# Kernel tuning notes

Measured on AMD Instinct MI355X. Metric: run time of the kernel, lower is better.

## Reference

```python
import jax, jax.numpy as jnp
import numpy as np
from jax import lax

B, N, NPOINT, NSAMPLE = 8, 8192, 2048, 32
RADIUS = 0.2
D_FEAT = 64
MLP = [64, 64, 128]
IN_CH = 3 + D_FEAT
EPS = 1e-5


def setup_inputs() -> dict:
    key = jax.random.key(0)
    ks = jax.random.split(key, 2 + len(MLP))
    inp = {
        "xyz": jax.random.uniform(ks[0], (B, N, 3), dtype=jnp.float32),
        "points": jax.random.normal(ks[1], (B, N, D_FEAT), dtype=jnp.float32),
    }
    cin = IN_CH
    for i, cout in enumerate(MLP):
        inp[f"W{i+1}"] = jax.random.normal(ks[2 + i], (cout, cin), dtype=jnp.float32) * 0.05
        inp[f"b{i+1}"] = jnp.zeros((cout,), jnp.float32)
        inp[f"g{i+1}"] = jnp.ones((cout,), jnp.float32)
        inp[f"be{i+1}"] = jnp.zeros((cout,), jnp.float32)
        cin = cout
    return inp


def farthest_point_sample(xyz, npoint):
    # xyz: (B, N, 3) -> (B, npoint) int32 indices. Deterministic start at index 0.
    Bb, Nn, _ = xyz.shape
    barange = jnp.arange(Bb)

    def step(carry, _):
        distance, farthest = carry
        centroid = xyz[barange, farthest]                      # (B, 3)
        d = jnp.sum((xyz - centroid[:, None, :]) ** 2, -1)     # (B, N)
        distance = jnp.minimum(distance, d)
        new_far = jnp.argmax(distance, axis=-1).astype(jnp.int32)
        return (distance, new_far), farthest

    init = (jnp.full((Bb, Nn), 1e10, xyz.dtype), jnp.zeros((Bb,), jnp.int32))
    _, idxs = lax.scan(step, init, None, length=npoint)        # (npoint, B)
    return idxs.T                                              # (B, npoint)


def index_points(points, idx):
    # points: (B, N, C); idx: (B, S) or (B, S, K)
    return jax.vmap(lambda p, i: p[i])(points, idx)


def square_distance(src, dst):
    # (B, S, C) x (B, N, C) -> (B, S, N)
    d = -2.0 * jnp.einsum('bsc,bnc->bsn', src, dst)
    d += jnp.sum(src ** 2, -1)[:, :, None]
    d += jnp.sum(dst ** 2, -1)[:, None, :]
    return d


def query_ball_point(radius, nsample, xyz, new_xyz):
    Bb, Nn, _ = xyz.shape
    sqr = square_distance(new_xyz, xyz)                        # (B, S, N)
    grid = jnp.arange(Nn, dtype=jnp.int32)
    group_idx = jnp.where(sqr > radius * radius, Nn, grid)     # invalid -> N
    # nsample smallest indices == torch sort(dim=-1)[:, :, :nsample]
    neg_vals, _ = lax.top_k(-group_idx, nsample)               # (B, S, K)
    group_idx = -neg_vals
    first = group_idx[:, :, 0:1]
    return jnp.where(group_idx == Nn, first, group_idx)


def bn_relu(x, gamma, beta):
    # x: (B, C, L). Training-mode batchnorm (biased variance) + ReLU.
    mean = jnp.mean(x, axis=(0, 2), keepdims=True)
    var = jnp.mean((x - mean) ** 2, axis=(0, 2), keepdims=True)
    xn = (x - mean) * lax.rsqrt(var + EPS)
    return jax.nn.relu(xn * gamma[None, :, None] + beta[None, :, None])


def reference(xyz, points, W1, b1, g1, be1, W2, b2, g2, be2, W3, b3, g3, be3):
    Bb = xyz.shape[0]
    fps_idx = farthest_point_sample(xyz, NPOINT)               # (B, S)
    new_xyz = index_points(xyz, fps_idx)                       # (B, S, 3)
    idx = query_ball_point(RADIUS, NSAMPLE, xyz, new_xyz)      # (B, S, K)
    grouped_xyz = index_points(xyz, idx)                       # (B, S, K, 3)
    grouped_xyz_norm = grouped_xyz - new_xyz[:, :, None, :]
    grouped_points = index_points(points, idx)                 # (B, S, K, D)
    g = jnp.concatenate([grouped_xyz_norm, grouped_points], -1)  # (B, S, K, C)
    x = g.reshape(Bb, NPOINT * NSAMPLE, -1).transpose(0, 2, 1)   # (B, C, S*K)
    for W, b, ga, be in ((W1, b1, g1, be1), (W2, b2, g2, be2), (W3, b3, g3, be3)):
        x = jnp.einsum('oc,bcl->bol', W, x) + b[None, :, None]
        x = bn_relu(x, ga, be)
    x = x.reshape(Bb, -1, NPOINT, NSAMPLE)
    new_points = jnp.max(x, axis=-1).transpose(0, 2, 1)        # (B, S, C_out)
    return new_xyz, new_points
```

## Files before the change

kernel.cpp:

```cpp
#include <hip/hip_runtime.h>
#include <hip/hip_bf16.h>

#define NB 8
#define NN 8192
#define NP 2048
#define NS 32
#define INV_P (1.0f/524288.0f)

typedef float v2f __attribute__((ext_vector_type(2)));

template<int CTRL>
__device__ __forceinline__ float fmax_dpp(float v) {
  const int x = __builtin_amdgcn_update_dpp(0, __float_as_int(v), CTRL, 0xF, 0xF, true);
  return fmaxf(v, __int_as_float(x));
}


__global__ __launch_bounds__(512)
void k_fps_pre(const float* __restrict__ xyz, const float* __restrict__ feat,
               const float* __restrict__ W1, const float* __restrict__ b1,
               float* __restrict__ F, float* __restrict__ outXyz, float* __restrict__ stats)
{
#pragma clang fp contract(off)
  __shared__ union U { float4 xyzw[NN]; float fx[128*64]; } sh;
  __shared__ unsigned long long cand[2][8];
  const int t = threadIdx.x;
  if (blockIdx.x < 8) {
    const int b = blockIdx.x;
    const float* xb = xyz + (size_t)b*NN*3;
    v2f px[8], py[8], pz[8], dd[8];
#pragma unroll
    for (int j = 0; j < 8; ++j) {
      const int i0 = t*16 + 2*j;
      const float x0 = xb[i0*3+0], y0 = xb[i0*3+1], z0 = xb[i0*3+2];
      const float x1 = xb[i0*3+3], y1 = xb[i0*3+4], z1 = xb[i0*3+5];
      px[j] = (v2f){x0,x1}; py[j] = (v2f){y0,y1}; pz[j] = (v2f){z0,z1};
      dd[j] = (v2f){1e10f,1e10f};
      sh.xyzw[i0]   = make_float4(x0,y0,z0,0.f);
      sh.xyzw[i0+1] = make_float4(x1,y1,z1,0.f);
    }
    __syncthreads();
    const int lane = t & 63, wv = t >> 6;
    float4 cf = sh.xyzw[0];
    for (int s = 0; s < NP; ++s) {
      if (t == 0) {
        float* o = outXyz + ((size_t)b*NP+s)*3;
        o[0]=cf.x; o[1]=cf.y; o[2]=cf.z;
      }
      const v2f cx = {cf.x,cf.x}, cy = {cf.y,cf.y}, cz = {cf.z,cf.z};
      float m = -1.f; int mi = 0;
#pragma unroll
      for (int j = 0; j < 8; ++j) {
        const v2f dx = px[j]-cx, dy = py[j]-cy, dz = pz[j]-cz;
        v2f d = dx*dx; d = d + dy*dy; d = d + dz*dz;
        const float n0 = fminf(dd[j].x, d.x);
        const float n1 = fminf(dd[j].y, d.y);
        dd[j].x = n0; dd[j].y = n1;
        if (n0 > m) { m = n0; mi = 2*j;   }
        if (n1 > m) { m = n1; mi = 2*j+1; }
      }
      float r = m;
      r = fmax_dpp<0xB1>(r);
      r = fmax_dpp<0x4E>(r);
      r = fmax_dpp<0x141>(r);
      r = fmax_dpp<0x140>(r);
      r = fmax_dpp<0x142>(r);
      r = fmax_dpp<0x143>(r);
      const int wmb  = __builtin_amdgcn_readlane(__float_as_int(r), 63);
      const float wm = __int_as_float(wmb);
      const unsigned long long mk = __ballot(m == wm);
      const int ls  = __ffsll((long long)mk) - 1;
      const int miw = __builtin_amdgcn_readlane(mi, ls);
      const unsigned idx = (unsigned)((wv*64 + ls)*16 + miw);
      if (lane == 0)
        cand[s&1][wv] = ((unsigned long long)(unsigned)wmb << 32)
                      | (unsigned long long)(0xFFFFFFFFu - idx);
      __syncthreads();
      unsigned long long best = cand[s&1][0];
#pragma unroll
      for (int w = 1; w < 8; ++w) { const unsigned long long c = cand[s&1][w]; if (c > best) best = c; }
      const int far = (int)(0xFFFFFFFFu - (unsigned)(best & 0xFFFFFFFFull));
      cf = sh.xyzw[far];
    }
  } else {
    if (blockIdx.x == 8) {
      for (int i = t; i < 512*16; i += 512) stats[i] = 0.f;
    }
    const int blk = blockIdx.x - 8;
    const int base = blk * 128;
    const int b = base >> 13;
    const int n0 = base & (NN-1);
    {
      const int row = t >> 2, seg = t & 3;
      const float* src = feat + ((size_t)(b*NN + n0 + row))*64 + seg*16;
#pragma unroll
      for (int k = 0; k < 4; ++k) {
        const float4 v = *(const float4*)(src + k*4);
        *(float4*)&sh.fx[row*64 + seg*16 + k*4] = v;
      }
    }
    __syncthreads();
    const int o = t & 63, wv = t >> 6;
    float w[64];
#pragma unroll
    for (int c = 0; c < 64; ++c) w[c] = W1[o*67 + 3 + c];
    const float bb = b1[o];
    for (int r = wv*16; r < wv*16+16; ++r) {
      float acc = bb;
#pragma unroll
      for (int c4 = 0; c4 < 16; ++c4) {
        const float4 xq = *(const float4*)&sh.fx[r*64 + c4*4];
        acc = fmaf(w[c4*4+0], xq.x, acc);
        acc = fmaf(w[c4*4+1], xq.y, acc);
        acc = fmaf(w[c4*4+2], xq.z, acc);
        acc = fmaf(w[c4*4+3], xq.w, acc);
      }
      F[((size_t)(b*NN + n0 + r))*64 + o] = acc;
    }
  }
}

__global__ __launch_bounds__(256)
void k_ball(const float* __restrict__ xyz, const float* __restrict__ newXyz,
            const float* __restrict__ F, const float* __restrict__ W1,
            __hip_bfloat16* __restrict__ y1, float* __restrict__ stats)
{
  __shared__ float xs[NN], ys[NN], zs[NN];
  __shared__ int sel[4][NS];
  const int t = threadIdx.x;
  const int b = blockIdx.x >> 5;
  const int chunk = blockIdx.x & 31;
  const float* xb = xyz + (size_t)b*NN*3;
  for (int i = t; i < NN; i += 256) {
    xs[i] = xb[i*3+0]; ys[i] = xb[i*3+1]; zs[i] = xb[i*3+2];
  }
  __syncthreads();
  const int lane = t & 63, wv = t >> 6;
  const float w0 = W1[lane*67+0], w1 = W1[lane*67+1], w2 = W1[lane*67+2];
  const double rr = 0.2*0.2;
  float ls = 0.f, lq = 0.f;
  for (int qi = 0; qi < 16; ++qi) {
    const int q  = chunk*64 + wv*16 + qi;
    const int gq = b*NP + q;
    const float cx = newXyz[(size_t)gq*3+0], cy = newXyz[(size_t)gq*3+1], cz = newXyz[(size_t)gq*3+2];
    const double cxd = (double)cx, cyd = (double)cy, czd = (double)cz;
    const double ssd = cxd*cxd + cyd*cyd + czd*czd;
    int have = 0;
    for (int c0 = 0; c0 < NN; c0 += 64) {
      const int i = c0 + lane;
      const double x = (double)xs[i], y = (double)ys[i], z = (double)zs[i];
      const double dot = x*cxd + y*cyd + z*czd;
      const double pn2 = x*x + y*y + z*z;
      const double d = -2.0*dot + ssd + pn2;
      const bool ok = d <= rr;
      const unsigned long long mk = __ballot(ok);
      const int rank = __popcll(mk & ((1ull<<lane)-1ull));
      if (ok && have + rank < NS) sel[wv][have+rank] = i;
      have += (int)__popcll(mk);
      if (have >= NS) break;
    }
    if (have > NS) have = NS;
    const int first = sel[wv][0];
    if (lane >= have && lane < NS) sel[wv][lane] = first;
    for (int j = 0; j < NS; ++j) {
      const int i = sel[wv][j];
      const float dxn = xs[i]-cx, dyn = ys[i]-cy, dzn = zs[i]-cz;
      const float f = F[((size_t)(b*NN+i))*64 + lane];
      float yv = fmaf(w0,dxn,f); yv = fmaf(w1,dyn,yv); yv = fmaf(w2,dzn,yv);
      y1[((size_t)gq*NS + j)*64 + lane] = __float2bfloat16(yv);
      ls += yv; lq = fmaf(yv,yv,lq);
    }
  }
  atomicAdd(&stats[(0 +lane)*16], ls);
  atomicAdd(&stats[(64+lane)*16], lq);
}

__device__ inline void stage_bn(const __hip_bfloat16* __restrict__ src, float* __restrict__ xt,
                                const float* __restrict__ A, const float* __restrict__ Bc,
                                int t, int blockBase)
{
  const uint4* s = (const uint4*)(src + ((size_t)(blockBase + t))*64);
  float* row = &xt[t*64];
  const int sw = t & 7;
#pragma unroll
  for (int g = 0; g < 8; ++g) {
    const uint4 v = s[g];
    const unsigned uu[4] = {v.x, v.y, v.z, v.w};
    const float4 Aq0 = ((const float4*)A)[g*2],  Aq1 = ((const float4*)A)[g*2+1];
    const float4 Bq0 = ((const float4*)Bc)[g*2], Bq1 = ((const float4*)Bc)[g*2+1];
    float e[8];
#pragma unroll
    for (int k = 0; k < 4; ++k) {
      const float f0 = __uint_as_float(uu[k] << 16);
      const float f1 = __uint_as_float(uu[k] & 0xFFFF0000u);
      const float a0 = (k<2) ? ((k==0)?Aq0.x:Aq0.z) : ((k==2)?Aq1.x:Aq1.z);
      const float a1 = (k<2) ? ((k==0)?Aq0.y:Aq0.w) : ((k==2)?Aq1.y:Aq1.w);
      const float bb0 = (k<2) ? ((k==0)?Bq0.x:Bq0.z) : ((k==2)?Bq1.x:Bq1.z);
      const float bb1 = (k<2) ? ((k==0)?Bq0.y:Bq0.w) : ((k==2)?Bq1.y:Bq1.w);
      e[k*2+0] = fmaxf(fmaf(f0, a0, bb0), 0.f);
      e[k*2+1] = fmaxf(fmaf(f1, a1, bb1), 0.f);
    }
    const float4 q0 = make_float4(e[0],e[1],e[2],e[3]);
    const float4 q1 = make_float4(e[4],e[5],e[6],e[7]);
    ((float4*)row)[(g*2)   ^ sw] = q0;
    ((float4*)row)[(g*2+1) ^ sw] = q1;
  }
}

__global__ __launch_bounds__(256)
void k_l2(const __hip_bfloat16* __restrict__ y1, float* __restrict__ stats,
          const float* __restrict__ g1, const float* __restrict__ be1,
          const float* __restrict__ W2, const float* __restrict__ b2,
          __hip_bfloat16* __restrict__ y2)
{
  __shared__ float xt[256*64];
  __shared__ float A[64], Bc[64], ssh[64], qsh[64];
  const int t = threadIdx.x;
  if (t < 64) {
    const float mean = stats[t*16] * INV_P;
    float var = stats[(64+t)*16] * INV_P - mean*mean;
    if (var < 0.f) var = 0.f;
    const float rs = rsqrtf(var + 1e-5f);
    const float a = rs * g1[t];
    A[t] = a; Bc[t] = fmaf(-mean, a, be1[t]);
    ssh[t] = 0.f; qsh[t] = 0.f;
  }
  const int lane = t & 63, wv = t >> 6;
  float w[64];
#pragma unroll
  for (int c4 = 0; c4 < 16; ++c4) {
    const float4 v = *(const float4*)(W2 + lane*64 + c4*4);
    w[c4*4+0]=v.x; w[c4*4+1]=v.y; w[c4*4+2]=v.z; w[c4*4+3]=v.w;
  }
  const float bo = b2[lane];
  __syncthreads();
  stage_bn(y1, xt, A, Bc, t, blockIdx.x*256);
  __syncthreads();
  float ls = 0.f, lq = 0.f;
  for (int pp = 0; pp < 64; ++pp) {
    const int p = wv*64 + pp;
    const int sw = p & 7;
    const float* row = &xt[p*64];
    float acc = bo;
#pragma unroll
    for (int c4 = 0; c4 < 16; ++c4) {
      const float4 xq = ((const float4*)row)[c4 ^ sw];
      acc = fmaf(w[c4*4+0], xq.x, acc);
      acc = fmaf(w[c4*4+1], xq.y, acc);
      acc = fmaf(w[c4*4+2], xq.z, acc);
      acc = fmaf(w[c4*4+3], xq.w, acc);
    }
    y2[((size_t)(blockIdx.x*256 + p))*64 + lane] = __float2bfloat16(acc);
    ls += acc; lq = fmaf(acc,acc,lq);
  }
  atomicAdd(&ssh[lane], ls);
  atomicAdd(&qsh[lane], lq);
  __syncthreads();
  if (t < 64) {
    atomicAdd(&stats[(128+t)*16], ssh[t]);
    atomicAdd(&stats[(192+t)*16], qsh[t]);
  }
}

__global__ __launch_bounds__(256)
void k_l3stats(const __hip_bfloat16* __restrict__ y2, float* __restrict__ stats,
               const float* __restrict__ g2, const float* __restrict__ be2,
               const float* __restrict__ W3, const float* __restrict__ b3)
{
  __shared__ float xt[256*64];
  __shared__ float A[64], Bc[64], ssh[128], qsh[128];
  const int t = threadIdx.x;
  if (t < 64) {
    const float mean = stats[(128+t)*16] * INV_P;
    float var = stats[(192+t)*16] * INV_P - mean*mean;
    if (var < 0.f) var = 0.f;
    const float rs = rsqrtf(var + 1e-5f);
    const float a = rs * g2[t];
    A[t] = a; Bc[t] = fmaf(-mean, a, be2[t]);
  }
  if (t < 128) { ssh[t]=0.f; qsh[t]=0.f; }
  const int lane = t & 63, wv = t >> 6;
  float w0[64], w1[64];
#pragma unroll
  for (int c4 = 0; c4 < 16; ++c4) {
    const float4 v  = *(const float4*)(W3 + lane*64 + c4*4);
    const float4 v2 = *(const float4*)(W3 + (size_t)(lane+64)*64 + c4*4);
    w0[c4*4+0]=v.x;  w0[c4*4+1]=v.y;  w0[c4*4+2]=v.z;  w0[c4*4+3]=v.w;
    w1[c4*4+0]=v2.x; w1[c4*4+1]=v2.y; w1[c4*4+2]=v2.z; w1[c4*4+3]=v2.w;
  }
  const float bo0 = b3[lane], bo1 = b3[lane+64];
  __syncthreads();
  stage_bn(y2, xt, A, Bc, t, blockIdx.x*256);
  __syncthreads();
  float ls0=0.f,lq0=0.f,ls1=0.f,lq1=0.f;
  for (int pp = 0; pp < 64; ++pp) {
    const int p = wv*64 + pp;
    const int sw = p & 7;
    const float* row = &xt[p*64];
    float a0 = bo0, a1 = bo1;
#pragma unroll
    for (int c4 = 0; c4 < 16; ++c4) {
      const float4 xq = ((const float4*)row)[c4 ^ sw];
      a0 = fmaf(w0[c4*4+0], xq.x, a0); a0 = fmaf(w0[c4*4+1], xq.y, a0);
      a0 = fmaf(w0[c4*4+2], xq.z, a0); a0 = fmaf(w0[c4*4+3], xq.w, a0);
      a1 = fmaf(w1[c4*4+0], xq.x, a1); a1 = fmaf(w1[c4*4+1], xq.y, a1);
      a1 = fmaf(w1[c4*4+2], xq.z, a1); a1 = fmaf(w1[c4*4+3], xq.w, a1);
    }
    ls0 += a0; lq0 = fmaf(a0,a0,lq0);
    ls1 += a1; lq1 = fmaf(a1,a1,lq1);
  }
  atomicAdd(&ssh[lane], ls0);    atomicAdd(&qsh[lane], lq0);
  atomicAdd(&ssh[64+lane], ls1); atomicAdd(&qsh[64+lane], lq1);
  __syncthreads();
  if (t < 128) {
    atomicAdd(&stats[(256+t)*16], ssh[t]);
    atomicAdd(&stats[(384+t)*16], qsh[t]);
  }
}

__global__ __launch_bounds__(256)
void k_out(const __hip_bfloat16* __restrict__ y2, const float* __restrict__ stats,
           const float* __restrict__ g2, const float* __restrict__ be2,
           const float* __restrict__ W3, const float* __restrict__ b3,
           const float* __restrict__ g3, const float* __restrict__ be3,
           float* __restrict__ out)
{
  __shared__ float xt[256*64];
  __shared__ float A[64], Bc[64], A3[128], B3[128];
  const int t = threadIdx.x;
  if (t < 64) {
    const float mean = stats[(128+t)*16] * INV_P;
    float var = stats[(192+t)*16] * INV_P - mean*mean;
    if (var < 0.f) var = 0.f;
    const float rs = rsqrtf(var + 1e-5f);
    const float a = rs * g2[t];
    A[t] = a; Bc[t] = fmaf(-mean, a, be2[t]);
  }
  if (t < 128) {
    const float mean = stats[(256+t)*16] * INV_P;
    float var = stats[(384+t)*16] * INV_P - mean*mean;
    if (var < 0.f) var = 0.f;
    const float rs = rsqrtf(var + 1e-5f);
    const float a = rs * g3[t];
    A3[t] = a; B3[t] = fmaf(-mean, a, be3[t]);
  }
  const int lane = t & 63, wv = t >> 6;
  float w0[64], w1[64];
#pragma unroll
  for (int c4 = 0; c4 < 16; ++c4) {
    const float4 v  = *(const float4*)(W3 + lane*64 + c4*4);
    const float4 v2 = *(const float4*)(W3 + (size_t)(lane+64)*64 + c4*4);
    w0[c4*4+0]=v.x;  w0[c4*4+1]=v.y;  w0[c4*4+2]=v.z;  w0[c4*4+3]=v.w;
    w1[c4*4+0]=v2.x; w1[c4*4+1]=v2.y; w1[c4*4+2]=v2.z; w1[c4*4+3]=v2.w;
  }
  const float bo0 = b3[lane], bo1 = b3[lane+64];
  __syncthreads();
  stage_bn(y2, xt, A, Bc, t, blockIdx.x*256);
  __syncthreads();
  const float a3l0 = A3[lane], b3l0 = B3[lane];
  const float a3l1 = A3[64+lane], b3l1 = B3[64+lane];
  for (int which = 0; which < 2; ++which) {
    float mx0 = -1e30f, mx1 = -1e30f;
    for (int j = 0; j < 32; ++j) {
      const int p = (wv*2+which)*32 + j;
      const int sw = p & 7;
      const float* row = &xt[p*64];
      float a0 = bo0, a1 = bo1;
#pragma unroll
      for (int c4 = 0; c4 < 16; ++c4) {
        const float4 xq = ((const float4*)row)[c4 ^ sw];
        a0 = fmaf(w0[c4*4+0], xq.x, a0); a0 = fmaf(w0[c4*4+1], xq.y, a0);
        a0 = fmaf(w0[c4*4+2], xq.z, a0); a0 = fmaf(w0[c4*4+3], xq.w, a0);
        a1 = fmaf(w1[c4*4+0], xq.x, a1); a1 = fmaf(w1[c4*4+1], xq.y, a1);
        a1 = fmaf(w1[c4*4+2], xq.z, a1); a1 = fmaf(w1[c4*4+3], xq.w, a1);
      }
      mx0 = fmaxf(mx0, fmaf(a0, a3l0, b3l0));
      mx1 = fmaxf(mx1, fmaf(a1, a3l1, b3l1));
    }
    const size_t gq = (size_t)blockIdx.x*8 + wv*2 + which;
    out[49152 + gq*128 + lane]      = fmaxf(mx0, 0.f);
    out[49152 + gq*128 + 64 + lane] = fmaxf(mx1, 0.f);
  }
}

extern "C" void kernel_launch(void* const* d_in, const int* in_sizes, int n_in,
                              void* d_out, int out_size, void* d_ws, size_t ws_size,
                              hipStream_t stream)
{
  const float* xyz = (const float*)d_in[0];
  const float* pts = (const float*)d_in[1];
  const float* W1  = (const float*)d_in[2];
  const float* b1  = (const float*)d_in[3];
  const float* g1  = (const float*)d_in[4];
  const float* be1 = (const float*)d_in[5];
  const float* W2  = (const float*)d_in[6];
  const float* b2_ = (const float*)d_in[7];
  const float* g2  = (const float*)d_in[8];
  const float* be2 = (const float*)d_in[9];
  const float* W3  = (const float*)d_in[10];
  const float* b3_ = (const float*)d_in[11];
  const float* g3  = (const float*)d_in[12];
  const float* be3 = (const float*)d_in[13];
  float* out = (float*)d_out;
  char* ws = (char*)d_ws;

  float* stats = (float*)(ws);
  float* F     = (float*)(ws + (1u<<20));
  __hip_bfloat16* y1 = (__hip_bfloat16*)(ws + (32u<<20));
  __hip_bfloat16* y2 = (__hip_bfloat16*)(ws + (112u<<20));

  k_fps_pre<<<520, 512, 0, stream>>>(xyz, pts, W1, b1, F, out, stats);
  k_ball<<<256, 256, 0, stream>>>(xyz, out, F, W1, y1, stats);
  k_l2<<<2048, 256, 0, stream>>>(y1, stats, g1, be1, W2, b2_, y2);
  k_l3stats<<<2048, 256, 0, stream>>>(y2, stats, g2, be2, W3, b3_);
  k_out<<<2048, 256, 0, stream>>>(y2, stats, g2, be2, W3, b3_, g3, be3, out);
}
```

Measured before the change: 2.375 ms.

## Use 1024-thread FPS blocks with shared atomicMax argmax reduction

The farthest-point-sampling block grows from 512 to 1024 threads, so each thread keeps 8 points instead of 16. The cross-wave argmax now uses a 64-bit atomicMax into a triple-buffered shared slot, which replaces the per-wave candidate array and the serial 8-way scan. The per-point index tracking in the hot loop is replaced by a recompute pass in the winning lane only. The feature-precompute branch is retiled to 256 rows per block to match the larger block, which also doubles per-block LDS for that path and halves the number of those blocks.

```diff
diff --git a/kernel.cpp b/kernel.cpp
--- a/kernel.cpp
+++ b/kernel.cpp
@@ -16,22 +16,22 @@
 }
 
 
-__global__ __launch_bounds__(512)
+__global__ __launch_bounds__(1024)
 void k_fps_pre(const float* __restrict__ xyz, const float* __restrict__ feat,
                const float* __restrict__ W1, const float* __restrict__ b1,
                float* __restrict__ F, float* __restrict__ outXyz, float* __restrict__ stats)
 {
 #pragma clang fp contract(off)
-  __shared__ union U { float4 xyzw[NN]; float fx[128*64]; } sh;
-  __shared__ unsigned long long cand[2][8];
+  __shared__ union U { float4 xyzw[NN]; float fx[256*64]; } sh;
+  __shared__ unsigned long long best[3];
   const int t = threadIdx.x;
   if (blockIdx.x < 8) {
     const int b = blockIdx.x;
     const float* xb = xyz + (size_t)b*NN*3;
-    v2f px[8], py[8], pz[8], dd[8];
-#pragma unroll
-    for (int j = 0; j < 8; ++j) {
-      const int i0 = t*16 + 2*j;
+    v2f px[4], py[4], pz[4], dd[4];
+#pragma unroll
+    for (int j = 0; j < 4; ++j) {
+      const int i0 = t*8 + 2*j;
       const float x0 = xb[i0*3+0], y0 = xb[i0*3+1], z0 = xb[i0*3+2];
       const float x1 = xb[i0*3+3], y1 = xb[i0*3+4], z1 = xb[i0*3+5];
       px[j] = (v2f){x0,x1}; py[j] = (v2f){y0,y1}; pz[j] = (v2f){z0,z1};
@@ -39,25 +39,27 @@
       sh.xyzw[i0]   = make_float4(x0,y0,z0,0.f);
       sh.xyzw[i0+1] = make_float4(x1,y1,z1,0.f);
     }
+    if (t == 0) { best[0] = 0ull; best[1] = 0ull; best[2] = 0ull; }
     __syncthreads();
-    const int lane = t & 63, wv = t >> 6;
+    const int lane = t & 63;
     float4 cf = sh.xyzw[0];
+    int rot = 0;
     for (int s = 0; s < NP; ++s) {
       if (t == 0) {
         float* o = outXyz + ((size_t)b*NP+s)*3;
         o[0]=cf.x; o[1]=cf.y; o[2]=cf.z;
       }
       const v2f cx = {cf.x,cf.x}, cy = {cf.y,cf.y}, cz = {cf.z,cf.z};
-      float m = -1.f; int mi = 0;
-#pragma unroll
-      for (int j = 0; j < 8; ++j) {
+      float m = -1.f;
+#pragma unroll
+      for (int j = 0; j < 4; ++j) {
         const v2f dx = px[j]-cx, dy = py[j]-cy, dz = pz[j]-cz;
         v2f d = dx*dx; d = d + dy*dy; d = d + dz*dz;
-        const float n0 = fminf(dd[j].x, d.x);
-        const float n1 = fminf(dd[j].y, d.y);
-        dd[j].x = n0; dd[j].y = n1;
-        if (n0 > m) { m = n0; mi = 2*j;   }
-        if (n1 > m) { m = n1; mi = 2*j+1; }
+        v2f nd;
+        nd.x = fminf(dd[j].x, d.x);
+        nd.y = fminf(dd[j].y, d.y);
+        dd[j] = nd;
+        m = fmaxf(m, fmaxf(nd.x, nd.y));
       }
       float r = m;
       r = fmax_dpp<0xB1>(r);
@@ -69,25 +71,33 @@
       const int wmb  = __builtin_amdgcn_readlane(__float_as_int(r), 63);
       const float wm = __int_as_float(wmb);
       const unsigned long long mk = __ballot(m == wm);
-      const int ls  = __ffsll((long long)mk) - 1;
-      const int miw = __builtin_amdgcn_readlane(mi, ls);
-      const unsigned idx = (unsigned)((wv*64 + ls)*16 + miw);
-      if (lane == 0)
-        cand[s&1][wv] = ((unsigned long long)(unsigned)wmb << 32)
-                      | (unsigned long long)(0xFFFFFFFFu - idx);
+      const int ls = __ffsll((long long)mk) - 1;
+      if (lane == ls) {
+        int k = 0;
+#pragma unroll
+        for (int j = 3; j >= 0; --j) {
+          if (dd[j].y == wm) k = 2*j+1;
+          if (dd[j].x == wm) k = 2*j;
+        }
+        const unsigned idx = (unsigned)(t*8 + k);
+        const unsigned long long pk = ((unsigned long long)(unsigned)wmb << 32)
+                                    | (unsigned long long)(0xFFFFFFFFu - idx);
+        atomicMax(&best[rot], pk);
+      }
+      const int nrot = (rot == 2) ? 0 : rot + 1;
+      if (t == 0) best[nrot] = 0ull;
       __syncthreads();
-      unsigned long long best = cand[s&1][0];
-#pragma unroll
-      for (int w = 1; w < 8; ++w) { const unsigned long long c = cand[s&1][w]; if (c > best) best = c; }
-      const int far = (int)(0xFFFFFFFFu - (unsigned)(best & 0xFFFFFFFFull));
+      const unsigned long long w = best[rot];
+      const int far = (int)(0xFFFFFFFFu - (unsigned)(w & 0xFFFFFFFFull));
       cf = sh.xyzw[far];
+      rot = nrot;
     }
   } else {
     if (blockIdx.x == 8) {
-      for (int i = t; i < 512*16; i += 512) stats[i] = 0.f;
+      for (int i = t; i < 512*16; i += 1024) stats[i] = 0.f;
     }
     const int blk = blockIdx.x - 8;
-    const int base = blk * 128;
+    const int base = blk * 256;
     const int b = base >> 13;
     const int n0 = base & (NN-1);
     {
@@ -409,7 +419,7 @@
   __hip_bfloat16* y1 = (__hip_bfloat16*)(ws + (32u<<20));
   __hip_bfloat16* y2 = (__hip_bfloat16*)(ws + (112u<<20));
 
-  k_fps_pre<<<520, 512, 0, stream>>>(xyz, pts, W1, b1, F, out, stats);
+  k_fps_pre<<<264, 1024, 0, stream>>>(xyz, pts, W1, b1, F, out, stats);
   k_ball<<<256, 256, 0, stream>>>(xyz, out, F, W1, y1, stats);
   k_l2<<<2048, 256, 0, stream>>>(y1, stats, g1, be1, W2, b2_, y2);
   k_l3stats<<<2048, 256, 0, stream>>>(y2, stats, g2, be2, W3, b3_);
```

Result: slower. 2.613 ms (+10.0%).

## Pack two FPS batches per block and fetch centroids from global memory

Applied to the files above, without the earlier changes.

The farthest-point-sampling part now processes two batches per 512-thread block, with 256 threads per batch each holding 32 points in registers, instead of one batch per block with 16 points per thread. The shared-memory xyz copy is dropped and each step's chosen centroid is read directly from global memory (likely L1/L2 resident). This halves the number of FPS blocks and shrinks shared memory, but each batch now has half the threads and does twice the per-thread serial work per step. The two batches also share one block-wide barrier per step, and the centroid load now goes through the global cache path instead of LDS.

```diff
diff --git a/kernel.cpp b/kernel.cpp
--- a/kernel.cpp
+++ b/kernel.cpp
@@ -22,35 +22,35 @@
                float* __restrict__ F, float* __restrict__ outXyz, float* __restrict__ stats)
 {
 #pragma clang fp contract(off)
-  __shared__ union U { float4 xyzw[NN]; float fx[128*64]; } sh;
+  __shared__ float fx[128*64];
   __shared__ unsigned long long cand[2][8];
   const int t = threadIdx.x;
-  if (blockIdx.x < 8) {
-    const int b = blockIdx.x;
+  if (blockIdx.x < 4) {
+    const int grp = t >> 8;
+    const int b   = blockIdx.x*2 + grp;
+    const int tg  = t & 255;
+    const int lane = t & 63;
+    const int wig  = (t >> 6) & 3;
     const float* xb = xyz + (size_t)b*NN*3;
-    v2f px[8], py[8], pz[8], dd[8];
-#pragma unroll
-    for (int j = 0; j < 8; ++j) {
-      const int i0 = t*16 + 2*j;
-      const float x0 = xb[i0*3+0], y0 = xb[i0*3+1], z0 = xb[i0*3+2];
-      const float x1 = xb[i0*3+3], y1 = xb[i0*3+4], z1 = xb[i0*3+5];
-      px[j] = (v2f){x0,x1}; py[j] = (v2f){y0,y1}; pz[j] = (v2f){z0,z1};
+    v2f px[16], py[16], pz[16], dd[16];
+#pragma unroll
+    for (int j = 0; j < 16; ++j) {
+      const int i0 = tg*32 + 2*j;
+      px[j] = (v2f){xb[i0*3+0], xb[i0*3+3]};
+      py[j] = (v2f){xb[i0*3+1], xb[i0*3+4]};
+      pz[j] = (v2f){xb[i0*3+2], xb[i0*3+5]};
       dd[j] = (v2f){1e10f,1e10f};
-      sh.xyzw[i0]   = make_float4(x0,y0,z0,0.f);
-      sh.xyzw[i0+1] = make_float4(x1,y1,z1,0.f);
-    }
-    __syncthreads();
-    const int lane = t & 63, wv = t >> 6;
-    float4 cf = sh.xyzw[0];
+    }
+    float cfx = xb[0], cfy = xb[1], cfz = xb[2];
     for (int s = 0; s < NP; ++s) {
-      if (t == 0) {
+      if (tg == 0) {
         float* o = outXyz + ((size_t)b*NP+s)*3;
-        o[0]=cf.x; o[1]=cf.y; o[2]=cf.z;
+        o[0]=cfx; o[1]=cfy; o[2]=cfz;
       }
-      const v2f cx = {cf.x,cf.x}, cy = {cf.y,cf.y}, cz = {cf.z,cf.z};
+      const v2f cx = {cfx,cfx}, cy = {cfy,cfy}, cz = {cfz,cfz};
       float m = -1.f; int mi = 0;
 #pragma unroll
-      for (int j = 0; j < 8; ++j) {
+      for (int j = 0; j < 16; ++j) {
         const v2f dx = px[j]-cx, dy = py[j]-cy, dz = pz[j]-cz;
         v2f d = dx*dx; d = d + dy*dy; d = d + dz*dz;
         const float n0 = fminf(dd[j].x, d.x);
@@ -71,22 +71,25 @@
       const unsigned long long mk = __ballot(m == wm);
       const int ls  = __ffsll((long long)mk) - 1;
       const int miw = __builtin_amdgcn_readlane(mi, ls);
-      const unsigned idx = (unsigned)((wv*64 + ls)*16 + miw);
+      const unsigned idx = (unsigned)((wig*64 + ls)*32 + miw);
       if (lane == 0)
-        cand[s&1][wv] = ((unsigned long long)(unsigned)wmb << 32)
-                      | (unsigned long long)(0xFFFFFFFFu - idx);
+        cand[s&1][t>>6] = ((unsigned long long)(unsigned)wmb << 32)
+                        | (unsigned long long)(0xFFFFFFFFu - idx);
       __syncthreads();
-      unsigned long long best = cand[s&1][0];
-#pragma unroll
-      for (int w = 1; w < 8; ++w) { const unsigned long long c = cand[s&1][w]; if (c > best) best = c; }
-      const int far = (int)(0xFFFFFFFFu - (unsigned)(best & 0xFFFFFFFFull));
-      cf = sh.xyzw[far];
+      const int buf = s & 1, base4 = grp*4;
+      const unsigned long long k0 = cand[buf][base4+0], k1 = cand[buf][base4+1];
+      const unsigned long long k2 = cand[buf][base4+2], k3 = cand[buf][base4+3];
+      const unsigned long long a0 = k0 > k1 ? k0 : k1;
+      const unsigned long long a1 = k2 > k3 ? k2 : k3;
+      const unsigned long long bk = a0 > a1 ? a0 : a1;
+      const int far = (int)(0xFFFFFFFFu - (unsigned)(bk & 0xFFFFFFFFull));
+      cfx = xb[far*3+0]; cfy = xb[far*3+1]; cfz = xb[far*3+2];
     }
   } else {
-    if (blockIdx.x == 8) {
+    if (blockIdx.x == 4) {
       for (int i = t; i < 512*16; i += 512) stats[i] = 0.f;
     }
-    const int blk = blockIdx.x - 8;
+    const int blk = blockIdx.x - 4;
     const int base = blk * 128;
     const int b = base >> 13;
     const int n0 = base & (NN-1);
@@ -96,7 +99,7 @@
 #pragma unroll
       for (int k = 0; k < 4; ++k) {
         const float4 v = *(const float4*)(src + k*4);
-        *(float4*)&sh.fx[row*64 + seg*16 + k*4] = v;
+        *(float4*)&fx[row*64 + seg*16 + k*4] = v;
       }
     }
     __syncthreads();
@@ -109,7 +112,7 @@
       float acc = bb;
 #pragma unroll
       for (int c4 = 0; c4 < 16; ++c4) {
-        const float4 xq = *(const float4*)&sh.fx[r*64 + c4*4];
+        const float4 xq = *(const float4*)&fx[r*64 + c4*4];
         acc = fmaf(w[c4*4+0], xq.x, acc);
         acc = fmaf(w[c4*4+1], xq.y, acc);
         acc = fmaf(w[c4*4+2], xq.z, acc);
@@ -409,7 +412,7 @@
   __hip_bfloat16* y1 = (__hip_bfloat16*)(ws + (32u<<20));
   __hip_bfloat16* y2 = (__hip_bfloat16*)(ws + (112u<<20));
 
-  k_fps_pre<<<520, 512, 0, stream>>>(xyz, pts, W1, b1, F, out, stats);
+  k_fps_pre<<<516, 512, 0, stream>>>(xyz, pts, W1, b1, F, out, stats);
   k_ball<<<256, 256, 0, stream>>>(xyz, out, F, W1, y1, stats);
   k_l2<<<2048, 256, 0, stream>>>(y1, stats, g1, be1, W2, b2_, y2);
   k_l3stats<<<2048, 256, 0, stream>>>(y2, stats, g2, be2, W3, b3_);
```

Result: slower. 3.787 ms (+59.4%).

## Fuse layer-3 stats with per-group max/min to skip recomputing the layer-3 GEMM

Applied to the files above, without the earlier changes.

The layer-3 kernel now records the per-group max and min of the pre-BN activations while it accumulates the batch-norm statistics. A light elementwise kernel then applies the affine BN transform, picking max or min depending on the sign of the scale, followed by ReLU. This relies on BN plus ReLU being monotone per channel, and it removes the second full pass over y2 and the repeated 64x128 matmul. The cost is two extra 8 MB buffers and one extra small launch.

```diff
diff --git a/kernel.cpp b/kernel.cpp
--- a/kernel.cpp
+++ b/kernel.cpp
@@ -263,9 +263,10 @@
 }
 
 __global__ __launch_bounds__(256)
-void k_l3stats(const __hip_bfloat16* __restrict__ y2, float* __restrict__ stats,
-               const float* __restrict__ g2, const float* __restrict__ be2,
-               const float* __restrict__ W3, const float* __restrict__ b3)
+void k_l3(const __hip_bfloat16* __restrict__ y2, float* __restrict__ stats,
+          const float* __restrict__ g2, const float* __restrict__ be2,
+          const float* __restrict__ W3, const float* __restrict__ b3,
+          float* __restrict__ mxbuf, float* __restrict__ mnbuf)
 {
   __shared__ float xt[256*64];
   __shared__ float A[64], Bc[64], ssh[128], qsh[128];
@@ -293,74 +294,8 @@
   stage_bn(y2, xt, A, Bc, t, blockIdx.x*256);
   __syncthreads();
   float ls0=0.f,lq0=0.f,ls1=0.f,lq1=0.f;
-  for (int pp = 0; pp < 64; ++pp) {
-    const int p = wv*64 + pp;
-    const int sw = p & 7;
-    const float* row = &xt[p*64];
-    float a0 = bo0, a1 = bo1;
-#pragma unroll
-    for (int c4 = 0; c4 < 16; ++c4) {
-      const float4 xq = ((const float4*)row)[c4 ^ sw];
-      a0 = fmaf(w0[c4*4+0], xq.x, a0); a0 = fmaf(w0[c4*4+1], xq.y, a0);
-      a0 = fmaf(w0[c4*4+2], xq.z, a0); a0 = fmaf(w0[c4*4+3], xq.w, a0);
-      a1 = fmaf(w1[c4*4+0], xq.x, a1); a1 = fmaf(w1[c4*4+1], xq.y, a1);
-      a1 = fmaf(w1[c4*4+2], xq.z, a1); a1 = fmaf(w1[c4*4+3], xq.w, a1);
-    }
-    ls0 += a0; lq0 = fmaf(a0,a0,lq0);
-    ls1 += a1; lq1 = fmaf(a1,a1,lq1);
-  }
-  atomicAdd(&ssh[lane], ls0);    atomicAdd(&qsh[lane], lq0);
-  atomicAdd(&ssh[64+lane], ls1); atomicAdd(&qsh[64+lane], lq1);
-  __syncthreads();
-  if (t < 128) {
-    atomicAdd(&stats[(256+t)*16], ssh[t]);
-    atomicAdd(&stats[(384+t)*16], qsh[t]);
-  }
-}
-
-__global__ __launch_bounds__(256)
-void k_out(const __hip_bfloat16* __restrict__ y2, const float* __restrict__ stats,
-           const float* __restrict__ g2, const float* __restrict__ be2,
-           const float* __restrict__ W3, const float* __restrict__ b3,
-           const float* __restrict__ g3, const float* __restrict__ be3,
-           float* __restrict__ out)
-{
-  __shared__ float xt[256*64];
-  __shared__ float A[64], Bc[64], A3[128], B3[128];
-  const int t = threadIdx.x;
-  if (t < 64) {
-    const float mean = stats[(128+t)*16] * INV_P;
-    float var = stats[(192+t)*16] * INV_P - mean*mean;
-    if (var < 0.f) var = 0.f;
-    const float rs = rsqrtf(var + 1e-5f);
-    const float a = rs * g2[t];
-    A[t] = a; Bc[t] = fmaf(-mean, a, be2[t]);
-  }
-  if (t < 128) {
-    const float mean = stats[(256+t)*16] * INV_P;
-    float var = stats[(384+t)*16] * INV_P - mean*mean;
-    if (var < 0.f) var = 0.f;
-    const float rs = rsqrtf(var + 1e-5f);
-    const float a = rs * g3[t];
-    A3[t] = a; B3[t] = fmaf(-mean, a, be3[t]);
-  }
-  const int lane = t & 63, wv = t >> 6;
-  float w0[64], w1[64];
-#pragma unroll
-  for (int c4 = 0; c4 < 16; ++c4) {
-    const float4 v  = *(const float4*)(W3 + lane*64 + c4*4);
-    const float4 v2 = *(const float4*)(W3 + (size_t)(lane+64)*64 + c4*4);
-    w0[c4*4+0]=v.x;  w0[c4*4+1]=v.y;  w0[c4*4+2]=v.z;  w0[c4*4+3]=v.w;
-    w1[c4*4+0]=v2.x; w1[c4*4+1]=v2.y; w1[c4*4+2]=v2.z; w1[c4*4+3]=v2.w;
-  }
-  const float bo0 = b3[lane], bo1 = b3[lane+64];
-  __syncthreads();
-  stage_bn(y2, xt, A, Bc, t, blockIdx.x*256);
-  __syncthreads();
-  const float a3l0 = A3[lane], b3l0 = B3[lane];
-  const float a3l1 = A3[64+lane], b3l1 = B3[64+lane];
   for (int which = 0; which < 2; ++which) {
-    float mx0 = -1e30f, mx1 = -1e30f;
+    float mx0 = -1e30f, mx1 = -1e30f, mn0 = 1e30f, mn1 = 1e30f;
     for (int j = 0; j < 32; ++j) {
       const int p = (wv*2+which)*32 + j;
       const int sw = p & 7;
@@ -374,13 +309,39 @@
         a1 = fmaf(w1[c4*4+0], xq.x, a1); a1 = fmaf(w1[c4*4+1], xq.y, a1);
         a1 = fmaf(w1[c4*4+2], xq.z, a1); a1 = fmaf(w1[c4*4+3], xq.w, a1);
       }
-      mx0 = fmaxf(mx0, fmaf(a0, a3l0, b3l0));
-      mx1 = fmaxf(mx1, fmaf(a1, a3l1, b3l1));
+      ls0 += a0; lq0 = fmaf(a0,a0,lq0);
+      ls1 += a1; lq1 = fmaf(a1,a1,lq1);
+      mx0 = fmaxf(mx0, a0); mn0 = fminf(mn0, a0);
+      mx1 = fmaxf(mx1, a1); mn1 = fminf(mn1, a1);
     }
     const size_t gq = (size_t)blockIdx.x*8 + wv*2 + which;
-    out[49152 + gq*128 + lane]      = fmaxf(mx0, 0.f);
-    out[49152 + gq*128 + 64 + lane] = fmaxf(mx1, 0.f);
-  }
+    mxbuf[gq*128 + lane]      = mx0;  mnbuf[gq*128 + lane]      = mn0;
+    mxbuf[gq*128 + 64 + lane] = mx1;  mnbuf[gq*128 + 64 + lane] = mn1;
+  }
+  atomicAdd(&ssh[lane], ls0);    atomicAdd(&qsh[lane], lq0);
+  atomicAdd(&ssh[64+lane], ls1); atomicAdd(&qsh[64+lane], lq1);
+  __syncthreads();
+  if (t < 128) {
+    atomicAdd(&stats[(256+t)*16], ssh[t]);
+    atomicAdd(&stats[(384+t)*16], qsh[t]);
+  }
+}
+
+__global__ __launch_bounds__(256)
+void k_out2(const float* __restrict__ mxbuf, const float* __restrict__ mnbuf,
+            const float* __restrict__ stats, const float* __restrict__ g3,
+            const float* __restrict__ be3, float* __restrict__ out)
+{
+  const int idx = blockIdx.x*256 + threadIdx.x;
+  const int ch = idx & 127;
+  const float mean = stats[(256+ch)*16] * INV_P;
+  float var = stats[(384+ch)*16] * INV_P - mean*mean;
+  if (var < 0.f) var = 0.f;
+  const float rs = rsqrtf(var + 1e-5f);
+  const float a = rs * g3[ch];
+  const float bc = fmaf(-mean, a, be3[ch]);
+  const float x = (a >= 0.f) ? mxbuf[idx] : mnbuf[idx];
+  out[49152 + idx] = fmaxf(fmaf(a, x, bc), 0.f);
 }
 
 extern "C" void kernel_launch(void* const* d_in, const int* in_sizes, int n_in,
@@ -406,12 +367,14 @@
 
   float* stats = (float*)(ws);
   float* F     = (float*)(ws + (1u<<20));
+  float* mxbuf = (float*)(ws + (17u<<20));
+  float* mnbuf = (float*)(ws + (25u<<20));
   __hip_bfloat16* y1 = (__hip_bfloat16*)(ws + (32u<<20));
   __hip_bfloat16* y2 = (__hip_bfloat16*)(ws + (112u<<20));
 
   k_fps_pre<<<520, 512, 0, stream>>>(xyz, pts, W1, b1, F, out, stats);
   k_ball<<<256, 256, 0, stream>>>(xyz, out, F, W1, y1, stats);
   k_l2<<<2048, 256, 0, stream>>>(y1, stats, g1, be1, W2, b2_, y2);
-  k_l3stats<<<2048, 256, 0, stream>>>(y2, stats, g2, be2, W3, b3_);
-  k_out<<<2048, 256, 0, stream>>>(y2, stats, g2, be2, W3, b3_, g3, be3, out);
-}
+  k_l3<<<2048, 256, 0, stream>>>(y2, stats, g2, be2, W3, b3_, mxbuf, mnbuf);
+  k_out2<<<8192, 256, 0, stream>>>(mxbuf, mnbuf, stats, g3, be3, out);
+}
```

Result: faster. 2.246 ms, median of 2 (-5.4%).
